# Performance work log

Hardware: AMD Instinct MI355X
Metric: run time of the kernel (lower is better)

## Reference

```python
import jax, jax.numpy as jnp
import numpy as np

NUM_EMBEDDINGS = 1024
EMBEDDING_DIM = 64
COMMIT_COST = 0.25


def setup_inputs() -> dict:
    key = jax.random.key(0)
    k1, k2 = jax.random.split(key)
    latent = jax.random.normal(k1, (32, EMBEDDING_DIM, 32, 32), dtype=jnp.float32)
    embedding_weight = jax.random.normal(k2, (NUM_EMBEDDINGS, EMBEDDING_DIM), dtype=jnp.float32)
    return {"latent": latent, "embedding_weight": embedding_weight}


def reference(latent, embedding_weight):
    # rearrange 'b n j d -> b j d n'; n == embedding_dim
    lat = jnp.transpose(latent, (0, 2, 3, 1))  # [b, j, d, n]
    flat = lat.reshape(-1, EMBEDDING_DIM)      # [T, D]
    # squared-euclidean distances [T, K]
    distances = (
        jnp.sum(flat ** 2, axis=1, keepdims=True)
        + jnp.sum(embedding_weight ** 2, axis=1)
        - 2.0 * flat @ embedding_weight.T
    )
    idx = jnp.argmin(distances, axis=1)                         # [T]
    encodings = jax.nn.one_hot(idx, NUM_EMBEDDINGS, dtype=flat.dtype)  # [T, K]
    quantized_flat = embedding_weight[idx]                      # gather == encodings @ W
    quantized = quantized_flat.reshape(lat.shape)               # [b, j, d, n]

    e_latent_loss = jnp.mean((jax.lax.stop_gradient(quantized) - lat) ** 2)
    loss = COMMIT_COST * e_latent_loss

    # straight-through estimator
    quantized_st = lat + jax.lax.stop_gradient(quantized - lat)

    avg_probs = jnp.mean(encodings, axis=0)
    perplexity = jnp.exp(-jnp.sum(avg_probs * jnp.log(avg_probs + 1e-10)))

    # rearrange back 'b j d n -> b n j d'
    quantized_out = jnp.transpose(quantized_st, (0, 3, 1, 2))
    return quantized_out, loss, perplexity, encodings, distances
```

## Files before the change

### kernel.cpp

```cpp
#include <hip/hip_runtime.h>
#include <cfloat>

#define T_TOTAL 32768
#define DIM 64
#define KCODES 1024

static constexpr long long OFF_Q    = 0;
static constexpr long long OFF_LOSS = 2097152;
static constexpr long long OFF_PERP = 2097153;
static constexpr long long OFF_ENC  = 2097154;
static constexpr long long OFF_DIST = 2097154LL + 33554432LL;


#define AS1 __attribute__((address_space(1)))
#define AS3 __attribute__((address_space(3)))

__device__ __forceinline__ void gld16(const float* g, float* l) {
    __builtin_amdgcn_global_load_lds((const AS1 unsigned int*)g,
                                     (AS3 unsigned int*)l, 16, 0, 0);
}

__global__ __launch_bounds__(256) void vq_prep_kernel(const float* __restrict__ W,
                                                      float* __restrict__ ww,
                                                      float* __restrict__ WT,
                                                      float* __restrict__ out) {
    const int tid = threadIdx.x;
    const int b   = blockIdx.x;
    if (b < 256) {
        const int lane = tid & 63;
        const int code = b * 4 + (tid >> 6);
        float v = W[code * DIM + lane];
        float s = v * v;
        #pragma unroll
        for (int off = 32; off > 0; off >>= 1)
            s += __shfl_down(s, off, 64);
        if (lane == 0) ww[code] = s;
    } else if (b < 320) {
        const int n = b - 256;
        #pragma unroll
        for (int i = 0; i < 4; ++i) {
            int k = i * 256 + tid;
            WT[n * KCODES + k] = W[k * DIM + n];
        }
    } else {
        float* __restrict__ enc = out + OFF_ENC;
        float4* __restrict__ p4 = (float4*)(enc + 2);
        const float4 z4 = make_float4(0.f, 0.f, 0.f, 0.f);
        const long long slot0 = (long long)(b - 320) * 4096;
        #pragma unroll
        for (int i = 0; i < 16; ++i) {
            long long s = slot0 + i * 256 + tid;
            if (s < 8388607LL) p4[s] = z4;
        }
        if (b == 320 && tid == 0) {
            *(float2*)&enc[0]        = make_float2(0.f, 0.f);
            *(float2*)&enc[33554430] = make_float2(0.f, 0.f);
        }
    }
}

__global__ __launch_bounds__(256, 2) void vq_main_kernel(const float* __restrict__ lat,
                                                         const float* __restrict__ W,
                                                         const float* __restrict__ ww,
                                                         const float* __restrict__ WT,
                                                         float* __restrict__ out,
                                                         int* __restrict__ counts,
                                                         float* __restrict__ lossSum) {
    __shared__ float xT[64 * 64];
    __shared__ float wS[2][8 * 512];
    __shared__ float wwS[KCODES];
    __shared__ float xx[64];
    __shared__ int   selIdx[64];

    const int tid = threadIdx.x;
    const int tx  = tid & 31;
    const int ty  = tid >> 5;
    const int t0  = blockIdx.x * 64;
    const long long base = (long long)(t0 >> 10) * 65536 + (long long)(t0 & 1023);
    const int wbase = (tid & 192) * 4;

    #pragma unroll
    for (int i = 0; i < 4; ++i) {
        const int e = i * 256 + tid;
        gld16(&lat[base + (long long)(e >> 4) * 1024 + (e & 15) * 4],
              &xT[i * 1024 + wbase]);
    }
    #pragma unroll
    for (int i = 0; i < 4; ++i) {
        const int e = i * 256 + tid;
        gld16(&WT[(e >> 7) * KCODES + (e & 127) * 4],
              &wS[0][i * 1024 + wbase]);
    }
    *(float4*)&wwS[tid * 4] = *(const float4*)&ww[tid * 4];
    __syncthreads();

    if (tid < 64) {
        float s = 0.f;
        #pragma unroll 8
        for (int n = 0; n < 64; ++n) {
            float v = xT[n * 64 + tid];
            s = fmaf(v, v, s);
        }
        xx[tid] = s;
    }

    float minV[8];
    int   minI[8];
    #pragma unroll
    for (int r = 0; r < 8; ++r) { minV[r] = FLT_MAX; minI[r] = 0; }

    float acc[8][16];
    float* __restrict__ distOut = out + OFF_DIST;
    float* __restrict__ enc     = out + OFF_ENC;

    for (int p = 0; p < 16; ++p) {
        const int c   = p >> 3;
        const int q   = p & 7;
        const int buf = p & 1;

        if (p < 15) {
            const int pn = p + 1;
            const float* srcb = WT + (pn & 7) * (8 * KCODES) + (pn >> 3) * 512;
            float* dstb = &wS[pn & 1][0];
            #pragma unroll
            for (int i = 0; i < 4; ++i) {
                const int e = i * 256 + tid;
                gld16(&srcb[(e >> 7) * KCODES + (e & 127) * 4],
                      &dstb[i * 1024 + wbase]);
            }
        }

        if (q == 0) {
            #pragma unroll
            for (int r = 0; r < 8; ++r)
                #pragma unroll
                for (int k = 0; k < 16; ++k) acc[r][k] = 0.f;
        }

        #pragma unroll 2
        for (int nn = 0; nn < 8; ++nn) {
            const float* xrow = &xT[(q * 8 + nn) * 64];
            const float* wrow = &wS[buf][nn * 512];
            float4 a0 = *(const float4*)&xrow[ty * 4];
            float4 a1 = *(const float4*)&xrow[32 + ty * 4];
            float4 b0 = *(const float4*)&wrow[tx * 4];
            float4 b1 = *(const float4*)&wrow[128 + tx * 4];
            float4 b2 = *(const float4*)&wrow[256 + tx * 4];
            float4 b3 = *(const float4*)&wrow[384 + tx * 4];
            float ar[8]  = {a0.x, a0.y, a0.z, a0.w, a1.x, a1.y, a1.z, a1.w};
            float br[16] = {b0.x, b0.y, b0.z, b0.w, b1.x, b1.y, b1.z, b1.w,
                            b2.x, b2.y, b2.z, b2.w, b3.x, b3.y, b3.z, b3.w};
            #pragma unroll
            for (int r = 0; r < 8; ++r)
                #pragma unroll
                for (int k = 0; k < 16; ++k)
                    acc[r][k] = fmaf(ar[r], br[k], acc[r][k]);
        }

        if (q == 7) {
            const int kb = c * 512 + tx * 4;
            float wr[16];
            #pragma unroll
            for (int qq = 0; qq < 4; ++qq) {
                float4 w4 = *(const float4*)&wwS[kb + qq * 128];
                wr[qq*4+0] = w4.x; wr[qq*4+1] = w4.y; wr[qq*4+2] = w4.z; wr[qq*4+3] = w4.w;
            }
            #pragma unroll
            for (int r = 0; r < 8; ++r) {
                const int row = (r >> 2) * 32 + ty * 4 + (r & 3);
                const float xxr = xx[row];
                const long long ro = (long long)(t0 + row) * KCODES + kb;
                #pragma unroll
                for (int qq = 0; qq < 4; ++qq) {
                    float d0 = (xxr + wr[qq*4+0]) - 2.f * acc[r][qq*4+0];
                    float d1 = (xxr + wr[qq*4+1]) - 2.f * acc[r][qq*4+1];
                    float d2 = (xxr + wr[qq*4+2]) - 2.f * acc[r][qq*4+2];
                    float d3 = (xxr + wr[qq*4+3]) - 2.f * acc[r][qq*4+3];
                    const int k0 = kb + qq * 128;
                    if (d0 < minV[r]) { minV[r] = d0; minI[r] = k0;     }
                    if (d1 < minV[r]) { minV[r] = d1; minI[r] = k0 + 1; }
                    if (d2 < minV[r]) { minV[r] = d2; minI[r] = k0 + 2; }
                    if (d3 < minV[r]) { minV[r] = d3; minI[r] = k0 + 3; }
                    *(float2*)&distOut[ro + qq * 128]     = make_float2(d0, d1);
                    *(float2*)&distOut[ro + qq * 128 + 2] = make_float2(d2, d3);
                }
            }
        }
        __syncthreads();
    }

    float* wSf  = &wS[0][0];
    float* redV = wSf;
    int*   redI = (int*)(wSf + 64 * 33);
    #pragma unroll
    for (int r = 0; r < 8; ++r) {
        const int row = (r >> 2) * 32 + ty * 4 + (r & 3);
        redV[row * 33 + tx] = minV[r];
        redI[row * 33 + tx] = minI[r];
    }
    __syncthreads();
    if (tid < 64) {
        float best = redV[tid * 33];
        int   bi   = redI[tid * 33];
        #pragma unroll
        for (int s = 1; s < 32; ++s) {
            float v  = redV[tid * 33 + s];
            int   i2 = redI[tid * 33 + s];
            if (v < best || (v == best && i2 < bi)) { best = v; bi = i2; }
        }
        selIdx[tid] = bi;
        atomicAdd(&counts[bi], 1);
    }
    __syncthreads();

    float* qS = wSf;
    #pragma unroll
    for (int i = 0; i < 16; ++i) {
        int e   = i * 256 + tid;
        int row = e >> 6;
        int n   = e & 63;
        qS[row * 65 + n] = W[selIdx[row] * DIM + n];
    }
    __syncthreads();

    float ls = 0.f;
    #pragma unroll
    for (int i = 0; i < 4; ++i) {
        int e2  = i * 256 + tid;
        int n   = e2 >> 4;
        int tl0 = (e2 & 15) * 4;
        float q0 = qS[(tl0 + 0) * 65 + n];
        float q1 = qS[(tl0 + 1) * 65 + n];
        float q2 = qS[(tl0 + 2) * 65 + n];
        float q3 = qS[(tl0 + 3) * 65 + n];
        float x0 = xT[n * 64 + tl0 + 0];
        float x1 = xT[n * 64 + tl0 + 1];
        float x2 = xT[n * 64 + tl0 + 2];
        float x3 = xT[n * 64 + tl0 + 3];
        *(float4*)&out[OFF_Q + base + (long long)n * 1024 + tl0] = make_float4(q0, q1, q2, q3);
        float e0 = q0 - x0; ls = fmaf(e0, e0, ls);
        float e1 = q1 - x1; ls = fmaf(e1, e1, ls);
        float e2d = q2 - x2; ls = fmaf(e2d, e2d, ls);
        float e3 = q3 - x3; ls = fmaf(e3, e3, ls);
    }
    #pragma unroll
    for (int off = 32; off > 0; off >>= 1)
        ls += __shfl_down(ls, off, 64);
    if ((tid & 63) == 0) atomicAdd(lossSum, ls);

    if (tid < 64)
        enc[(long long)(t0 + tid) * KCODES + selIdx[tid]] = 1.f;
}

__global__ __launch_bounds__(1024) void vq_finalize_kernel(const int* __restrict__ counts,
                                                           const float* __restrict__ lossSum,
                                                           float* __restrict__ out) {
    __shared__ float red[16];
    const int tid = threadIdx.x;
    float p = (float)counts[tid] * (1.0f / 32768.0f);
    float term = p * logf(p + 1e-10f);
    #pragma unroll
    for (int off = 32; off > 0; off >>= 1)
        term += __shfl_down(term, off, 64);
    if ((tid & 63) == 0) red[tid >> 6] = term;
    __syncthreads();
    if (tid == 0) {
        float s = 0.f;
        #pragma unroll
        for (int i = 0; i < 16; ++i) s += red[i];
        out[OFF_PERP] = expf(-s);
        out[OFF_LOSS] = 0.25f * lossSum[0] * (1.0f / 2097152.0f);
    }
}

extern "C" void kernel_launch(void* const* d_in, const int* in_sizes, int n_in,
                              void* d_out, int out_size, void* d_ws, size_t ws_size,
                              hipStream_t stream) {
    (void)in_sizes; (void)n_in; (void)out_size; (void)ws_size;
    const float* lat = (const float*)d_in[0];
    const float* W   = (const float*)d_in[1];
    float* out = (float*)d_out;

    int*   counts  = (int*)d_ws;
    float* ww      = (float*)((char*)d_ws + 4096);
    float* lossSum = (float*)((char*)d_ws + 8192);
    float* WT      = (float*)((char*)d_ws + 12288);

    hipMemsetAsync(d_ws, 0, 8192 + 16, stream);

    vq_prep_kernel<<<2368, 256, 0, stream>>>(W, ww, WT, out);
    vq_main_kernel<<<512, 256, 0, stream>>>(lat, W, ww, WT, out, counts, lossSum);
    vq_finalize_kernel<<<1, 1024, 0, stream>>>(counts, lossSum, out);
}
```

Baseline: 352.2 us.

## Move encodings zero-fill into main kernel and relax per-phase barrier waits

```diff
diff --git a/kernel.cpp b/kernel.cpp
--- a/kernel.cpp
+++ b/kernel.cpp
@@ -20,10 +20,18 @@
                                      (AS3 unsigned int*)l, 16, 0, 0);
 }
 
+#define PHASE_SYNC(N) do {                                        \
+    asm volatile("s_waitcnt vmcnt(" #N ")" ::: "memory");         \
+    __builtin_amdgcn_s_barrier();                                 \
+    __builtin_amdgcn_sched_barrier(0);                            \
+} while (0)
+
 __global__ __launch_bounds__(256) void vq_prep_kernel(const float* __restrict__ W,
                                                       float* __restrict__ ww,
                                                       float* __restrict__ WT,
-                                                      float* __restrict__ out) {
+                                                      float* __restrict__ out,
+                                                      int* __restrict__ counts,
+                                                      float* __restrict__ lossSum) {
     const int tid = threadIdx.x;
     const int b   = blockIdx.x;
     if (b < 256) {
@@ -42,20 +50,19 @@
             int k = i * 256 + tid;
             WT[n * KCODES + k] = W[k * DIM + n];
         }
+    } else if (b < 384) {
+        float* __restrict__ enc = out + OFF_ENC;
+        const float2 z2 = make_float2(0.f, 0.f);
+        const int r0 = (b - 320) * 512 + tid * 2;
+        const long long rb = (long long)r0 * KCODES;
+        *(float2*)&enc[rb]               = z2;
+        *(float2*)&enc[rb + 1022]        = z2;
+        *(float2*)&enc[rb + 1024]        = z2;
+        *(float2*)&enc[rb + 1024 + 1022] = z2;
     } else {
-        float* __restrict__ enc = out + OFF_ENC;
-        float4* __restrict__ p4 = (float4*)(enc + 2);
-        const float4 z4 = make_float4(0.f, 0.f, 0.f, 0.f);
-        const long long slot0 = (long long)(b - 320) * 4096;
-        #pragma unroll
-        for (int i = 0; i < 16; ++i) {
-            long long s = slot0 + i * 256 + tid;
-            if (s < 8388607LL) p4[s] = z4;
-        }
-        if (b == 320 && tid == 0) {
-            *(float2*)&enc[0]        = make_float2(0.f, 0.f);
-            *(float2*)&enc[33554430] = make_float2(0.f, 0.f);
-        }
+        #pragma unroll
+        for (int i = 0; i < 4; ++i) counts[i * 256 + tid] = 0;
+        if (tid == 0) lossSum[0] = 0.f;
     }
 }
 
@@ -112,6 +119,8 @@
     float acc[8][16];
     float* __restrict__ distOut = out + OFF_DIST;
     float* __restrict__ enc     = out + OFF_ENC;
+    const float4 z4 = make_float4(0.f, 0.f, 0.f, 0.f);
+    const int tcl = (tid < 255 ? tid : 254) * 4;
 
     for (int p = 0; p < 16; ++p) {
         const int c   = p >> 3;
@@ -128,6 +137,15 @@
                 gld16(&srcb[(e >> 7) * KCODES + (e & 127) * 4],
                       &dstb[i * 1024 + wbase]);
             }
+        }
+        asm volatile("" ::: "memory");
+
+        {
+            float* pz = enc + (long long)(t0 + p * 4) * KCODES + 2;
+            *(float4*)(pz + tcl)        = z4;
+            *(float4*)(pz + 1024 + tcl) = z4;
+            *(float4*)(pz + 2048 + tcl) = z4;
+            *(float4*)(pz + 3072 + tcl) = z4;
         }
 
         if (q == 0) {
@@ -186,7 +204,9 @@
                 }
             }
         }
-        __syncthreads();
+
+        if (q == 7) PHASE_SYNC(63);
+        else        PHASE_SYNC(4);
     }
 
     float* wSf  = &wS[0][0];
@@ -286,9 +306,7 @@
     float* lossSum = (float*)((char*)d_ws + 8192);
     float* WT      = (float*)((char*)d_ws + 12288);
 
-    hipMemsetAsync(d_ws, 0, 8192 + 16, stream);
-
-    vq_prep_kernel<<<2368, 256, 0, stream>>>(W, ww, WT, out);
+    vq_prep_kernel<<<385, 256, 0, stream>>>(W, ww, WT, out, counts, lossSum);
     vq_main_kernel<<<512, 256, 0, stream>>>(lat, W, ww, WT, out, counts, lossSum);
     vq_finalize_kernel<<<1, 1024, 0, stream>>>(counts, lossSum, out);
 }
```

Measured after the change: 338.0 us. 1.04x faster.
